# Kernel tuning notes

Measured on AMD Instinct MI355X. Metric: run time of the kernel, lower is better.

Reference implementation:

```python
import jax, jax.numpy as jnp
import numpy as np

WSIZE = (12, 12)
NUM_HEADS = 12
HEAD_DIM = 64


def _rel_idx(ws):
    wh, ww = ws
    num_dist = (2 * wh - 1) * (2 * ww - 1) + 3
    coords = np.stack(np.meshgrid(np.arange(wh), np.arange(ww), indexing='ij'))
    coords = coords.reshape(2, -1)                       # [2, wh*ww]
    rel = (coords[:, :, None] - coords[:, None, :]).transpose(1, 2, 0)
    rel[:, :, 0] += wh - 1
    rel[:, :, 1] += ww - 1
    rel[:, :, 0] *= 2 * ww - 1
    idx = np.zeros((wh * ww + 1,) * 2, dtype=np.int32)
    idx[1:, 1:] = rel.sum(-1)
    idx[0, 0:] = num_dist - 3
    idx[0:, 0] = num_dist - 2
    idx[0, 0] = num_dist - 1
    return idx.flatten()                                  # [(wh*ww+1)**2]

REL_IDX = jnp.asarray(_rel_idx(WSIZE))


def setup_inputs() -> dict:
    key = jax.random.key(0)
    ks = jax.random.split(key, 8)
    B, S, D = 1024, WSIZE[0] * WSIZE[1] + 1, NUM_HEADS * HEAD_DIM
    num_dist = (2 * WSIZE[0] - 1) * (2 * WSIZE[1] - 1) + 3
    return {
        'x': jax.random.normal(ks[0], (B, S, D), jnp.float32),
        'attn_mask': jax.random.normal(ks[1], (B, 1, S, S), jnp.float32),
        'Wq': jax.random.normal(ks[2], (D, D), jnp.float32) * 0.02,
        'bq': jnp.zeros((D,), jnp.float32),
        'Wk': jax.random.normal(ks[3], (D, D), jnp.float32) * 0.02,
        'Wv': jax.random.normal(ks[4], (D, D), jnp.float32) * 0.02,
        'bv': jnp.zeros((D,), jnp.float32),
        'rel_bias_tbl': jax.random.normal(ks[5], (num_dist, NUM_HEADS), jnp.float32) * 0.02,
    }


def reference(x, attn_mask, Wq, bq, Wk, Wv, bv, rel_bias_tbl):
    B, S, _ = x.shape
    H, D = NUM_HEADS, HEAD_DIM

    def heads(e):  # [B,S,H*D] -> [B,H,S,D]
        return e.reshape(B, S, H, D).transpose(0, 2, 1, 3)

    q = heads(x @ Wq + bq)
    k = heads(x @ Wk)            # key has no bias
    v = heads(x @ Wv + bv)

    scores = jnp.einsum('bhqd,bhkd->bhqk', q, k) / np.sqrt(D).astype(x.dtype)
    scores = scores + attn_mask
    # relative position bias: gather [S*S, H] -> [S,S,H] -> [1,H,S,S]
    rel_bias = rel_bias_tbl[REL_IDX].reshape(S, S, H).transpose(2, 0, 1)[None]
    scores = scores + rel_bias

    probs = jax.nn.softmax(scores, axis=-1)
    ctx = jnp.einsum('bhqk,bhkd->bhqd', probs, v)          # [B,H,S,D]
    return ctx.transpose(0, 2, 1, 3).reshape(B, S, H * D)
```

## Files before the change

### kernel.cpp

```cpp
#include <hip/hip_runtime.h>
#include <hip/hip_bf16.h>

typedef __bf16 bf16x8 __attribute__((ext_vector_type(8)));
typedef float f32x4 __attribute__((ext_vector_type(4)));
typedef float f32x4u __attribute__((ext_vector_type(4), aligned(4)));

#define NH 12
#define HD 64
#define SEQ 145
#define SP 160
#define DMODEL 768
#define NTOT 2304
#define BDIM 1024
#define RBS 148

__device__ __forceinline__ ushort f2bf(float f) {
  union { float f; uint u; } a; a.f = f;
  uint u = a.u;
  return (ushort)((u + 0x7FFFu + ((u >> 16) & 1u)) >> 16);
}

__device__ __forceinline__ int relidx(int qi, int ki) {
  if (ki == 0) return (qi == 0) ? 531 : 530;
  if (qi == 0) return 529;
  int q = qi - 1, k = ki - 1;
  int qh = q / 12, qw = q - qh * 12;
  int kh = k / 12, kw = k - kh * 12;
  return (qh - kh + 11) * 23 + (qw - kw + 11);
}

__device__ __forceinline__ void gload_lds16(const ushort* g, ushort* l) {
  __builtin_amdgcn_global_load_lds(
      (const __attribute__((address_space(1))) void*)g,
      (__attribute__((address_space(3))) void*)l, 16, 0, 0);
}

#define VMCNT(n) do { asm volatile("s_waitcnt vmcnt(" #n ")" ::: "memory"); \
                      __builtin_amdgcn_sched_barrier(0); } while (0)

__global__ void prep_w(const float* __restrict__ Wq, const float* __restrict__ Wk,
                       const float* __restrict__ Wv, ushort* __restrict__ Wt) {
  int i = blockIdx.x * 256 + threadIdx.x;
  if (i >= NTOT * DMODEL) return;
  int n = i / DMODEL, k = i - n * DMODEL;
  const float* W = (n < DMODEL) ? Wq : (n < 2 * DMODEL ? Wk : Wv);
  int c = n % DMODEL;
  Wt[i] = f2bf(W[k * DMODEL + c]);
}

__global__ void x2bf(const float* __restrict__ x, ushort* __restrict__ xb) {
  const size_t total = (size_t)BDIM * SEQ * DMODEL;
  size_t i = ((size_t)blockIdx.x * 256 + threadIdx.x) * 8;
  if (i >= total) return;
  float4 a = *reinterpret_cast<const float4*>(x + i);
  float4 c = *reinterpret_cast<const float4*>(x + i + 4);
  uint4 o;
  o.x = (uint)f2bf(a.x) | ((uint)f2bf(a.y) << 16);
  o.y = (uint)f2bf(a.z) | ((uint)f2bf(a.w) << 16);
  o.z = (uint)f2bf(c.x) | ((uint)f2bf(c.y) << 16);
  o.w = (uint)f2bf(c.z) | ((uint)f2bf(c.w) << 16);
  *reinterpret_cast<uint4*>(xb + i) = o;
}

__global__ void zero_vpad(ushort* __restrict__ vbuf) {
  int i = blockIdx.x * 256 + threadIdx.x;
  const int total = BDIM * NH * HD * (SP - SEQ);
  if (i >= total) return;
  int s = SEQ + i % (SP - SEQ);
  int row = i / (SP - SEQ);
  vbuf[(size_t)row * SP + s] = 0;
}

__global__ void rel_prep(const float* __restrict__ tbl, float* __restrict__ rbias) {
  int i = blockIdx.x * 256 + threadIdx.x;
  if (i >= NH * SEQ * RBS) return;
  int h = i / (SEQ * RBS);
  int rem = i - h * SEQ * RBS;
  int qi = rem / RBS, ki = rem - qi * RBS;
  rbias[i] = (ki < SEQ) ? tbl[relidx(qi, ki) * NH + h] : 0.f;
}

#define GNT 9
#define GNWG 10440
#define NKT 24

__global__ __launch_bounds__(512, 4)
void qkv_gemm(const ushort* __restrict__ xb, const ushort* __restrict__ Wt,
              const float* __restrict__ bq, const float* __restrict__ bv,
              ushort* __restrict__ qbuf, ushort* __restrict__ kbuf,
              ushort* __restrict__ vbuf) {
  __shared__ __align__(16) ushort lds[36864];

  int bid = blockIdx.x;
  int logical = (bid & 7) * 1305 + (bid >> 3);
  int mt = logical / GNT, nt = logical - (logical / GNT) * GNT;
  int m0 = mt * 128, n0 = nt * 256;

  int tid = threadIdx.x;
  int l = tid & 63, w = tid >> 6;
  int wm = w >> 2, wn = w & 3;
  int l15 = l & 15, l4 = l >> 4;
  int rslot = l4 ^ ((l15 >> 1) & 3);

  int srow = tid >> 2;
  int schunk = (tid & 3) ^ ((tid >> 3) & 3);
  const ushort* aSrc  = xb + (size_t)(m0 + srow) * DMODEL + schunk * 8;
  const ushort* bSrc0 = Wt + (size_t)(n0 + srow) * DMODEL + schunk * 8;
  const ushort* bSrc1 = Wt + (size_t)(n0 + 128 + srow) * DMODEL + schunk * 8;
  int wdst = w << 9;

#define STAGE(db, kof) do { \
    gload_lds16(aSrc  + (kof), &lds[(db) * 4096 + wdst]); \
    gload_lds16(bSrc0 + (kof), &lds[12288 + (db) * 8192 + wdst]); \
    gload_lds16(bSrc1 + (kof), &lds[12288 + (db) * 8192 + 4096 + wdst]); \
  } while (0)

  f32x4 acc[4][4];
  #pragma unroll
  for (int m = 0; m < 4; m++)
    #pragma unroll
    for (int n = 0; n < 4; n++)
      #pragma unroll
      for (int e = 0; e < 4; e++) acc[m][n][e] = 0.f;

  bf16x8 af[4], bfv[4];

#define LOADFRAG(db) do { \
    int ab_ = (db) * 4096, bb_ = 12288 + (db) * 8192; \
    _Pragma("unroll") \
    for (int i_ = 0; i_ < 4; i_++) \
      af[i_] = *reinterpret_cast<const bf16x8*>( \
          &lds[ab_ + ((wm * 64 + i_ * 16 + l15) << 5) + rslot * 8]); \
    _Pragma("unroll") \
    for (int n_ = 0; n_ < 4; n_++) \
      bfv[n_] = *reinterpret_cast<const bf16x8*>( \
          &lds[bb_ + ((wn * 64 + n_ * 16 + l15) << 5) + rslot * 8]); \
  } while (0)
#define MFMA16() do { \
    __builtin_amdgcn_s_setprio(1); \
    _Pragma("unroll") \
    for (int i_ = 0; i_ < 4; i_++) \
      _Pragma("unroll") \
      for (int n_ = 0; n_ < 4; n_++) \
        acc[i_][n_] = __builtin_amdgcn_mfma_f32_16x16x32_bf16( \
            af[i_], bfv[n_], acc[i_][n_], 0, 0, 0); \
    __builtin_amdgcn_s_setprio(0); \
  } while (0)

  STAGE(0, 0);
  STAGE(1, 32);
  VMCNT(3);
  __builtin_amdgcn_s_barrier();

  #pragma unroll
  for (int t = 0; t < NKT; ++t) {
    int cur = t % 3, nx2 = (t + 2) % 3;
    if (t + 2 < NKT) STAGE(nx2, (t + 2) * 32);
    LOADFRAG(cur);
    MFMA16();
    if (t < NKT - 1) {
      if (t + 2 < NKT) { VMCNT(3); }
      else             { VMCNT(0); }
      __builtin_amdgcn_s_barrier();
    }
  }

  int which = n0 / DMODEL;
  int h_[4], dh_[4];
  float bias_[4];
  #pragma unroll
  for (int nn = 0; nn < 4; nn++) {
    int col = n0 + wn * 64 + nn * 16 + l15;
    int hcol = col - which * DMODEL;
    h_[nn] = hcol >> 6; dh_[nn] = hcol & 63;
    bias_[nn] = (which == 0) ? bq[hcol] : (which == 2 ? bv[hcol] : 0.f);
  }

  if (which != 2) {
    #pragma unroll
    for (int i = 0; i < 4; i++) {
      #pragma unroll
      for (int r = 0; r < 4; r++) {
        int row = m0 + wm * 64 + i * 16 + (l4 << 2) + r;
        int b = row / SEQ;
        int s = row - b * SEQ;
        #pragma unroll
        for (int nn = 0; nn < 4; nn++) {
          float v = acc[i][nn][r] + bias_[nn];
          size_t bh = (size_t)b * NH + h_[nn];
          if (which == 0) {
            v *= 0.125f;
            qbuf[(bh * SEQ + s) * HD + dh_[nn]] = f2bf(v);
          } else {
            kbuf[(bh * SEQ + s) * HD + dh_[nn]] = f2bf(v);
          }
        }
      }
    }
  } else {
    __syncthreads();
    ushort* T = &lds[w * 4608];
    #pragma unroll
    for (int i = 0; i < 4; i++) {
      #pragma unroll
      for (int nn = 0; nn < 4; nn++) {
        int cl = nn * 16 + l15;
        int rl = i * 16 + (l4 << 2);
        ushort4 pk;
        pk.x = f2bf(acc[i][nn][0] + bias_[nn]);
        pk.y = f2bf(acc[i][nn][1] + bias_[nn]);
        pk.z = f2bf(acc[i][nn][2] + bias_[nn]);
        pk.w = f2bf(acc[i][nn][3] + bias_[nn]);
        *reinterpret_cast<ushort4*>(&T[cl * 72 + rl]) = pk;
      }
    }
    asm volatile("s_waitcnt lgkmcnt(0)" ::: "memory");
    __builtin_amdgcn_sched_barrier(0);
    int hU = ((n0 - 2 * DMODEL) >> 6) + wn;
    int rowbase = m0 + wm * 64;
    #pragma unroll
    for (int c = 0; c < 8; c++) {
      uint4 vv = *reinterpret_cast<const uint4*>(&T[l * 72 + c * 8]);
      int R = rowbase + c * 8;
      int b0 = R / SEQ;
      int b7 = (R + 7) / SEQ;
      if (b0 == b7) {
        int s0 = R - b0 * SEQ;
        size_t addr = (((size_t)b0 * NH + hU) * HD + l) * SP + s0;
        *reinterpret_cast<uint4*>(vbuf + addr) = vv;
      } else {
        const ushort* pv = reinterpret_cast<const ushort*>(&vv);
        #pragma unroll
        for (int e = 0; e < 8; e++) {
          int row = R + e;
          int bb = row / SEQ, ss = row - bb * SEQ;
          vbuf[(((size_t)bb * NH + hU) * HD + l) * SP + ss] = pv[e];
        }
      }
    }
  }
#undef STAGE
#undef LOADFRAG
#undef MFMA16
}

#define AH 4
__global__ __launch_bounds__(256, 2)
void attn_kernel(const ushort* __restrict__ qbuf, const ushort* __restrict__ kbuf,
                 const ushort* __restrict__ vbuf, const float* __restrict__ mask,
                 const float* __restrict__ rbias, float* __restrict__ out) {
  __shared__ __align__(16) ushort plds[AH][16][SP + 8];

  int id = blockIdx.x;
  int xcd = id & 7;
  int j = id >> 3;
  int b = xcd + 8 * (j / 3);
  int hg = j % 3;

  int tid = threadIdx.x;
  int lane = tid & 63, w = tid >> 6;
  int h = hg * AH + w;
  int l15 = lane & 15, l4 = lane >> 4;
  int bh = b * NH + h;

  const ushort* qp = qbuf + (size_t)bh * SEQ * HD;
  const ushort* kp = kbuf + (size_t)bh * SEQ * HD;
  const ushort* vp = vbuf + (size_t)bh * HD * SP;
  const float* mbase = mask + (size_t)b * SEQ * SEQ;
  const float* rbase = rbias + (size_t)h * SEQ * RBS;

  uint4 kfa[10], kfb[10];
  #pragma unroll
  for (int ct = 0; ct < 5; ct++) {
    int krow = ct * 16 + l15;
    kfa[2 * ct]     = *reinterpret_cast<const uint4*>(kp + krow * HD + l4 * 8);
    kfa[2 * ct + 1] = *reinterpret_cast<const uint4*>(kp + krow * HD + 32 + l4 * 8);
  }
  #pragma unroll
  for (int ct = 5; ct < 10; ct++) {
    int krow = ct * 16 + l15;
    if (krow >= SEQ) krow = 0;
    kfb[2 * (ct - 5)]     = *reinterpret_cast<const uint4*>(kp + krow * HD + l4 * 8);
    kfb[2 * (ct - 5) + 1] = *reinterpret_cast<const uint4*>(kp + krow * HD + 32 + l4 * 8);
  }
  uint4 vba[10], vbb[10];
  #pragma unroll
  for (int t = 0; t < 10; t++) {
    int ntl = t / 5, ks = t % 5;
    vba[t] = *reinterpret_cast<const uint4*>(
        vp + (ntl * 16 + l15) * SP + ks * 32 + l4 * 8);
  }
  #pragma unroll
  for (int t = 0; t < 10; t++) {
    int ntl = 2 + t / 5, ks = t % 5;
    vbb[t] = *reinterpret_cast<const uint4*>(
        vp + (ntl * 16 + l15) * SP + ks * 32 + l4 * 8);
  }

  #pragma unroll 1
  for (int strip = 0; strip < 10; strip++) {
    int r0 = strip * 16;
    int qi = r0 + l15;
    int qc = (qi < SEQ) ? qi : (SEQ - 1);
    bool qok = (qi < SEQ);
    const float* mrow = mbase + (size_t)qc * SEQ;
    const float* rp = rbase + (size_t)qc * RBS;

    bf16x8 qf0, qf1;
    if (qok) {
      qf0 = *reinterpret_cast<const bf16x8*>(qp + qi * HD + l4 * 8);
      qf1 = *reinterpret_cast<const bf16x8*>(qp + qi * HD + 32 + l4 * 8);
    } else {
      uint4 z = make_uint4(0, 0, 0, 0);
      qf0 = *reinterpret_cast<bf16x8*>(&z);
      qf1 = *reinterpret_cast<bf16x8*>(&z);
    }

    f32x4 sc[10];
    #pragma unroll
    for (int ct = 0; ct < 9; ct++) {
      int kb = ct * 16 + l4 * 4;
      f32x4u rb = *reinterpret_cast<const f32x4u*>(rp + kb);
      f32x4u mk = *reinterpret_cast<const f32x4u*>(mrow + kb);
      #pragma unroll
      for (int r = 0; r < 4; r++)
        sc[ct][r] = qok ? (mk[r] + rb[r]) : -3e38f;
    }
    {
      float iv = (l4 == 0 && qok) ? (mrow[144] + rp[144]) : -3e38f;
      sc[9][0] = iv; sc[9][1] = -3e38f; sc[9][2] = -3e38f; sc[9][3] = -3e38f;
    }

    #pragma unroll
    for (int ct = 0; ct < 5; ct++) {
      sc[ct] = __builtin_amdgcn_mfma_f32_16x16x32_bf16(
          *reinterpret_cast<bf16x8*>(&kfa[2 * ct]), qf0, sc[ct], 0, 0, 0);
      sc[ct] = __builtin_amdgcn_mfma_f32_16x16x32_bf16(
          *reinterpret_cast<bf16x8*>(&kfa[2 * ct + 1]), qf1, sc[ct], 0, 0, 0);
    }
    #pragma unroll
    for (int ct = 5; ct < 10; ct++) {
      sc[ct] = __builtin_amdgcn_mfma_f32_16x16x32_bf16(
          *reinterpret_cast<bf16x8*>(&kfb[2 * (ct - 5)]), qf0, sc[ct], 0, 0, 0);
      sc[ct] = __builtin_amdgcn_mfma_f32_16x16x32_bf16(
          *reinterpret_cast<bf16x8*>(&kfb[2 * (ct - 5) + 1]), qf1, sc[ct], 0, 0, 0);
    }

    float mx = -3e38f;
    #pragma unroll
    for (int ct = 0; ct < 10; ct++)
      #pragma unroll
      for (int r = 0; r < 4; r++) mx = fmaxf(mx, sc[ct][r]);
    mx = fmaxf(mx, __shfl_xor(mx, 16, 64));
    mx = fmaxf(mx, __shfl_xor(mx, 32, 64));
    float sum = 0.f;
    #pragma unroll
    for (int ct = 0; ct < 10; ct++)
      #pragma unroll
      for (int r = 0; r < 4; r++) {
        float p = __expf(sc[ct][r] - mx);
        sc[ct][r] = p;
        sum += p;
      }
    sum += __shfl_xor(sum, 16, 64);
    sum += __shfl_xor(sum, 32, 64);
    float inv = 1.f / sum;

    #pragma unroll
    for (int ct = 0; ct < 10; ct++) {
      ushort4 pk;
      pk.x = f2bf(sc[ct][0] * inv);
      pk.y = f2bf(sc[ct][1] * inv);
      pk.z = f2bf(sc[ct][2] * inv);
      pk.w = f2bf(sc[ct][3] * inv);
      *reinterpret_cast<ushort4*>(&plds[w][l15][ct * 16 + l4 * 4]) = pk;
    }

    #pragma unroll
    for (int ntl = 0; ntl < 2; ntl++) {
      f32x4 pacc;
      #pragma unroll
      for (int e = 0; e < 4; e++) pacc[e] = 0.f;
      #pragma unroll
      for (int ks = 0; ks < 5; ks++) {
        bf16x8 pa = *reinterpret_cast<const bf16x8*>(
            &plds[w][l15][ks * 32 + l4 * 8]);
        pacc = __builtin_amdgcn_mfma_f32_16x16x32_bf16(
            pa, *reinterpret_cast<bf16x8*>(&vba[ntl * 5 + ks]), pacc, 0, 0, 0);
      }
      #pragma unroll
      for (int r = 0; r < 4; r++) {
        int s = r0 + l4 * 4 + r;
        if (s < SEQ)
          out[((size_t)b * SEQ + s) * DMODEL + h * HD + ntl * 16 + l15] = pacc[r];
      }
    }
    #pragma unroll
    for (int ntl = 2; ntl < 4; ntl++) {
      f32x4 pacc;
      #pragma unroll
      for (int e = 0; e < 4; e++) pacc[e] = 0.f;
      #pragma unroll
      for (int ks = 0; ks < 5; ks++) {
        bf16x8 pa = *reinterpret_cast<const bf16x8*>(
            &plds[w][l15][ks * 32 + l4 * 8]);
        pacc = __builtin_amdgcn_mfma_f32_16x16x32_bf16(
            pa, *reinterpret_cast<bf16x8*>(&vbb[(ntl - 2) * 5 + ks]), pacc, 0, 0, 0);
      }
      #pragma unroll
      for (int r = 0; r < 4; r++) {
        int s = r0 + l4 * 4 + r;
        if (s < SEQ)
          out[((size_t)b * SEQ + s) * DMODEL + h * HD + ntl * 16 + l15] = pacc[r];
      }
    }
  }
}

extern "C" void kernel_launch(void* const* d_in, const int* in_sizes, int n_in,
                              void* d_out, int out_size, void* d_ws, size_t ws_size,
                              hipStream_t stream) {
  const float* x    = (const float*)d_in[0];
  const float* mask = (const float*)d_in[1];
  const float* Wq   = (const float*)d_in[2];
  const float* bq   = (const float*)d_in[3];
  const float* Wk   = (const float*)d_in[4];
  const float* Wv   = (const float*)d_in[5];
  const float* bv   = (const float*)d_in[6];
  const float* tbl  = (const float*)d_in[7];
  float* out = (float*)d_out;

  char* ws = (char*)d_ws;
  ushort* Wt = (ushort*)ws;
  size_t off = (size_t)NTOT * DMODEL * 2;
  ushort* qbuf = (ushort*)(ws + off); off += (size_t)BDIM * NH * SEQ * HD * 2;
  ushort* kbuf = (ushort*)(ws + off); off += (size_t)BDIM * NH * SEQ * HD * 2;
  ushort* vbuf = (ushort*)(ws + off); off += (size_t)BDIM * NH * HD * SP * 2;
  float*  rbias = (float*)(ws + off); off += (size_t)NH * SEQ * RBS * 4 + 64;

  ushort* xbuf = (ushort*)d_out;

  prep_w<<<(NTOT * DMODEL + 255) / 256, 256, 0, stream>>>(Wq, Wk, Wv, Wt);
  zero_vpad<<<(BDIM * NH * HD * (SP - SEQ) + 255) / 256, 256, 0, stream>>>(vbuf);
  rel_prep<<<(NH * SEQ * RBS + 255) / 256, 256, 0, stream>>>(tbl, rbias);
  {
    size_t total = (size_t)BDIM * SEQ * DMODEL;
    x2bf<<<(int)(total / 8 / 256), 256, 0, stream>>>(x, xbuf);
  }

  qkv_gemm<<<GNWG, 512, 0, stream>>>(xbuf, Wt, bq, bv, qbuf, kbuf, vbuf);

  attn_kernel<<<BDIM * 3, 256, 0, stream>>>(qbuf, kbuf, vbuf, mask, rbias, out);
}
```

Before: 1.231 ms.

## Fuse fp32-to-bf16 conversion of x into the QKV GEMM A-tile loader

Removes the separate x2bf kernel and has the QKV GEMM read fp32 x directly. Each A tile is loaded into registers, converted to bf16 and written to LDS, double-buffered in registers across iterations, while B still uses direct global-to-LDS loads. This saves a full pass that writes and rereads the bf16 copy of x. In exchange, A is read as fp32 by each of the 9 N-tiles, doubling A traffic per workgroup, and the pipeline gains extra register pressure and an LDS wait before each barrier.

```diff
diff --git a/kernel.cpp b/kernel.cpp
--- a/kernel.cpp
+++ b/kernel.cpp
@@ -20,6 +20,10 @@
   return (ushort)((u + 0x7FFFu + ((u >> 16) & 1u)) >> 16);
 }
 
+__device__ __forceinline__ uint pk2(float lo, float hi) {
+  return (uint)f2bf(lo) | ((uint)f2bf(hi) << 16);
+}
+
 __device__ __forceinline__ int relidx(int qi, int ki) {
   if (ki == 0) return (qi == 0) ? 531 : 530;
   if (qi == 0) return 529;
@@ -37,6 +41,8 @@
 
 #define VMCNT(n) do { asm volatile("s_waitcnt vmcnt(" #n ")" ::: "memory"); \
                       __builtin_amdgcn_sched_barrier(0); } while (0)
+#define LGKM0 do { asm volatile("s_waitcnt lgkmcnt(0)" ::: "memory"); \
+                   __builtin_amdgcn_sched_barrier(0); } while (0)
 
 __global__ void prep_w(const float* __restrict__ Wq, const float* __restrict__ Wk,
                        const float* __restrict__ Wv, ushort* __restrict__ Wt) {
@@ -48,20 +54,6 @@
   Wt[i] = f2bf(W[k * DMODEL + c]);
 }
 
-__global__ void x2bf(const float* __restrict__ x, ushort* __restrict__ xb) {
-  const size_t total = (size_t)BDIM * SEQ * DMODEL;
-  size_t i = ((size_t)blockIdx.x * 256 + threadIdx.x) * 8;
-  if (i >= total) return;
-  float4 a = *reinterpret_cast<const float4*>(x + i);
-  float4 c = *reinterpret_cast<const float4*>(x + i + 4);
-  uint4 o;
-  o.x = (uint)f2bf(a.x) | ((uint)f2bf(a.y) << 16);
-  o.y = (uint)f2bf(a.z) | ((uint)f2bf(a.w) << 16);
-  o.z = (uint)f2bf(c.x) | ((uint)f2bf(c.y) << 16);
-  o.w = (uint)f2bf(c.z) | ((uint)f2bf(c.w) << 16);
-  *reinterpret_cast<uint4*>(xb + i) = o;
-}
-
 __global__ void zero_vpad(ushort* __restrict__ vbuf) {
   int i = blockIdx.x * 256 + threadIdx.x;
   const int total = BDIM * NH * HD * (SP - SEQ);
@@ -85,7 +77,7 @@
 #define NKT 24
 
 __global__ __launch_bounds__(512, 4)
-void qkv_gemm(const ushort* __restrict__ xb, const ushort* __restrict__ Wt,
+void qkv_gemm(const float* __restrict__ x, const ushort* __restrict__ Wt,
               const float* __restrict__ bq, const float* __restrict__ bv,
               ushort* __restrict__ qbuf, ushort* __restrict__ kbuf,
               ushort* __restrict__ vbuf) {
@@ -102,15 +94,26 @@
   int l15 = l & 15, l4 = l >> 4;
   int rslot = l4 ^ ((l15 >> 1) & 3);
 
-  int srow = tid >> 2;
+  int arow = tid >> 2;
+  const float* xf = x + (size_t)(m0 + arow) * DMODEL + (tid & 3) * 8;
+  int awaddr = (arow << 5) + (((tid & 3) ^ ((tid >> 3) & 3)) << 3);
+
   int schunk = (tid & 3) ^ ((tid >> 3) & 3);
-  const ushort* aSrc  = xb + (size_t)(m0 + srow) * DMODEL + schunk * 8;
-  const ushort* bSrc0 = Wt + (size_t)(n0 + srow) * DMODEL + schunk * 8;
-  const ushort* bSrc1 = Wt + (size_t)(n0 + 128 + srow) * DMODEL + schunk * 8;
+  const ushort* bSrc0 = Wt + (size_t)(n0 + arow) * DMODEL + schunk * 8;
+  const ushort* bSrc1 = Wt + (size_t)(n0 + 128 + arow) * DMODEL + schunk * 8;
   int wdst = w << 9;
 
-#define STAGE(db, kof) do { \
-    gload_lds16(aSrc  + (kof), &lds[(db) * 4096 + wdst]); \
+#define ALOAD(s0, s1, kof) do { \
+    s0 = *reinterpret_cast<const float4*>(xf + (kof)); \
+    s1 = *reinterpret_cast<const float4*>(xf + (kof) + 4); \
+  } while (0)
+#define ACVTW(db, s0, s1) do { \
+    uint4 o_; \
+    o_.x = pk2(s0.x, s0.y); o_.y = pk2(s0.z, s0.w); \
+    o_.z = pk2(s1.x, s1.y); o_.w = pk2(s1.z, s1.w); \
+    *reinterpret_cast<uint4*>(&lds[(db) * 4096 + awaddr]) = o_; \
+  } while (0)
+#define STAGE_B(db, kof) do { \
     gload_lds16(bSrc0 + (kof), &lds[12288 + (db) * 8192 + wdst]); \
     gload_lds16(bSrc1 + (kof), &lds[12288 + (db) * 8192 + 4096 + wdst]); \
   } while (0)
@@ -147,20 +150,33 @@
     __builtin_amdgcn_s_setprio(0); \
   } while (0)
 
-  STAGE(0, 0);
-  STAGE(1, 32);
-  VMCNT(3);
+  float4 aE0, aE1, aO0, aO1;
+
+  ALOAD(aE0, aE1, 0);
+  STAGE_B(0, 0);
+  ALOAD(aO0, aO1, 32);
+  STAGE_B(1, 32);
+  VMCNT(4);
+  ACVTW(0, aE0, aE1);
+  LGKM0;
   __builtin_amdgcn_s_barrier();
 
   #pragma unroll
   for (int t = 0; t < NKT; ++t) {
-    int cur = t % 3, nx2 = (t + 2) % 3;
-    if (t + 2 < NKT) STAGE(nx2, (t + 2) * 32);
-    LOADFRAG(cur);
+    if (t + 2 < NKT) {
+      if ((t & 1) == 0) ALOAD(aE0, aE1, (t + 2) * 32);
+      else              ALOAD(aO0, aO1, (t + 2) * 32);
+      STAGE_B((t + 2) % 3, (t + 2) * 32);
+    }
+    if (t + 1 < NKT) {
+      if (t + 2 < NKT) { VMCNT(4); } else { VMCNT(0); }
+      if ((t & 1) == 0) ACVTW((t + 1) % 3, aO0, aO1);
+      else              ACVTW((t + 1) % 3, aE0, aE1);
+    }
+    LOADFRAG(t % 3);
     MFMA16();
     if (t < NKT - 1) {
-      if (t + 2 < NKT) { VMCNT(3); }
-      else             { VMCNT(0); }
+      LGKM0;
       __builtin_amdgcn_s_barrier();
     }
   }
@@ -214,8 +230,7 @@
         *reinterpret_cast<ushort4*>(&T[cl * 72 + rl]) = pk;
       }
     }
-    asm volatile("s_waitcnt lgkmcnt(0)" ::: "memory");
-    __builtin_amdgcn_sched_barrier(0);
+    LGKM0;
     int hU = ((n0 - 2 * DMODEL) >> 6) + wn;
     int rowbase = m0 + wm * 64;
     #pragma unroll
@@ -239,7 +254,9 @@
       }
     }
   }
-#undef STAGE
+#undef ALOAD
+#undef ACVTW
+#undef STAGE_B
 #undef LOADFRAG
 #undef MFMA16
 }
@@ -438,17 +455,11 @@
   ushort* vbuf = (ushort*)(ws + off); off += (size_t)BDIM * NH * HD * SP * 2;
   float*  rbias = (float*)(ws + off); off += (size_t)NH * SEQ * RBS * 4 + 64;
 
-  ushort* xbuf = (ushort*)d_out;
-
   prep_w<<<(NTOT * DMODEL + 255) / 256, 256, 0, stream>>>(Wq, Wk, Wv, Wt);
   zero_vpad<<<(BDIM * NH * HD * (SP - SEQ) + 255) / 256, 256, 0, stream>>>(vbuf);
   rel_prep<<<(NH * SEQ * RBS + 255) / 256, 256, 0, stream>>>(tbl, rbias);
-  {
-    size_t total = (size_t)BDIM * SEQ * DMODEL;
-    x2bf<<<(int)(total / 8 / 256), 256, 0, stream>>>(x, xbuf);
-  }
-
-  qkv_gemm<<<GNWG, 512, 0, stream>>>(xbuf, Wt, bq, bv, qbuf, kbuf, vbuf);
+
+  qkv_gemm<<<GNWG, 512, 0, stream>>>(x, Wt, bq, bv, qbuf, kbuf, vbuf);
 
   attn_kernel<<<BDIM * 3, 256, 0, stream>>>(qbuf, kbuf, vbuf, mask, rbias, out);
 }
```

Result: slower. 1.344 ms (+9.2%).

## Merge prep kernels and stage Q/K epilogue through LDS for 16-byte stores

Applied to the files above, without the earlier changes.

Merges the weight transpose, V-padding zeroing and relative-bias table prep into one launch to cut kernel launch overhead. The Q/K GEMM epilogue now writes bf16 results into per-wave LDS tiles and then issues coalesced 16-byte global stores of 8 consecutive head-dim elements, replacing scattered 2-byte stores. This adds a block barrier and LDS traffic before the epilogue for all tiles.

```diff
diff --git a/kernel.cpp b/kernel.cpp
--- a/kernel.cpp
+++ b/kernel.cpp
@@ -38,14 +38,35 @@
 #define VMCNT(n) do { asm volatile("s_waitcnt vmcnt(" #n ")" ::: "memory"); \
                       __builtin_amdgcn_sched_barrier(0); } while (0)
 
-__global__ void prep_w(const float* __restrict__ Wq, const float* __restrict__ Wk,
-                       const float* __restrict__ Wv, ushort* __restrict__ Wt) {
-  int i = blockIdx.x * 256 + threadIdx.x;
-  if (i >= NTOT * DMODEL) return;
-  int n = i / DMODEL, k = i - n * DMODEL;
-  const float* W = (n < DMODEL) ? Wq : (n < 2 * DMODEL ? Wk : Wv);
-  int c = n % DMODEL;
-  Wt[i] = f2bf(W[k * DMODEL + c]);
+#define NP1 6912
+#define NP2 46080
+#define NP3 1006
+__global__ void prep_all(const float* __restrict__ Wq, const float* __restrict__ Wk,
+                         const float* __restrict__ Wv, ushort* __restrict__ Wt,
+                         ushort* __restrict__ vbuf, const float* __restrict__ tbl,
+                         float* __restrict__ rbias) {
+  int bid = blockIdx.x;
+  int tid = threadIdx.x;
+  if (bid < NP1) {
+    int i = bid * 256 + tid;
+    int n = i / DMODEL, k = i - n * DMODEL;
+    const float* W = (n < DMODEL) ? Wq : (n < 2 * DMODEL ? Wk : Wv);
+    int c = n % DMODEL;
+    Wt[i] = f2bf(W[k * DMODEL + c]);
+  } else if (bid < NP1 + NP2) {
+    int i = (bid - NP1) * 256 + tid;
+    int s = SEQ + i % (SP - SEQ);
+    int row = i / (SP - SEQ);
+    vbuf[(size_t)row * SP + s] = 0;
+  } else {
+    int i = (bid - NP1 - NP2) * 256 + tid;
+    if (i < NH * SEQ * RBS) {
+      int h = i / (SEQ * RBS);
+      int rem = i - h * SEQ * RBS;
+      int qi = rem / RBS, ki = rem - qi * RBS;
+      rbias[i] = (ki < SEQ) ? tbl[relidx(qi, ki) * NH + h] : 0.f;
+    }
+  }
 }
 
 __global__ void x2bf(const float* __restrict__ x, ushort* __restrict__ xb) {
@@ -60,24 +81,6 @@
   o.z = (uint)f2bf(c.x) | ((uint)f2bf(c.y) << 16);
   o.w = (uint)f2bf(c.z) | ((uint)f2bf(c.w) << 16);
   *reinterpret_cast<uint4*>(xb + i) = o;
-}
-
-__global__ void zero_vpad(ushort* __restrict__ vbuf) {
-  int i = blockIdx.x * 256 + threadIdx.x;
-  const int total = BDIM * NH * HD * (SP - SEQ);
-  if (i >= total) return;
-  int s = SEQ + i % (SP - SEQ);
-  int row = i / (SP - SEQ);
-  vbuf[(size_t)row * SP + s] = 0;
-}
-
-__global__ void rel_prep(const float* __restrict__ tbl, float* __restrict__ rbias) {
-  int i = blockIdx.x * 256 + threadIdx.x;
-  if (i >= NH * SEQ * RBS) return;
-  int h = i / (SEQ * RBS);
-  int rem = i - h * SEQ * RBS;
-  int qi = rem / RBS, ki = rem - qi * RBS;
-  rbias[i] = (ki < SEQ) ? tbl[relidx(qi, ki) * NH + h] : 0.f;
 }
 
 #define GNT 9
@@ -166,40 +169,43 @@
   }
 
   int which = n0 / DMODEL;
-  int h_[4], dh_[4];
   float bias_[4];
   #pragma unroll
   for (int nn = 0; nn < 4; nn++) {
     int col = n0 + wn * 64 + nn * 16 + l15;
     int hcol = col - which * DMODEL;
-    h_[nn] = hcol >> 6; dh_[nn] = hcol & 63;
     bias_[nn] = (which == 0) ? bq[hcol] : (which == 2 ? bv[hcol] : 0.f);
   }
+  int hU = ((n0 - which * DMODEL) >> 6) + wn;
+  int rowbase = m0 + wm * 64;
+
+  __syncthreads();
+  ushort* T = &lds[w * 4608];
 
   if (which != 2) {
-    #pragma unroll
-    for (int i = 0; i < 4; i++) {
-      #pragma unroll
-      for (int r = 0; r < 4; r++) {
-        int row = m0 + wm * 64 + i * 16 + (l4 << 2) + r;
-        int b = row / SEQ;
-        int s = row - b * SEQ;
+    float scale = (which == 0) ? 0.125f : 1.f;
+    #pragma unroll
+    for (int i = 0; i < 4; i++)
+      #pragma unroll
+      for (int nn = 0; nn < 4; nn++)
         #pragma unroll
-        for (int nn = 0; nn < 4; nn++) {
-          float v = acc[i][nn][r] + bias_[nn];
-          size_t bh = (size_t)b * NH + h_[nn];
-          if (which == 0) {
-            v *= 0.125f;
-            qbuf[(bh * SEQ + s) * HD + dh_[nn]] = f2bf(v);
-          } else {
-            kbuf[(bh * SEQ + s) * HD + dh_[nn]] = f2bf(v);
-          }
-        }
-      }
+        for (int r = 0; r < 4; r++)
+          T[(i * 16 + (l4 << 2) + r) * 72 + nn * 16 + l15] =
+              f2bf((acc[i][nn][r] + bias_[nn]) * scale);
+    asm volatile("s_waitcnt lgkmcnt(0)" ::: "memory");
+    __builtin_amdgcn_sched_barrier(0);
+    ushort* dst = (which == 0) ? qbuf : kbuf;
+    int chunk = l & 7;
+    #pragma unroll
+    for (int c = 0; c < 8; c++) {
+      int rl = (l >> 3) + 8 * c;
+      uint4 vv = *reinterpret_cast<const uint4*>(&T[rl * 72 + chunk * 8]);
+      int row = rowbase + rl;
+      int bb = row / SEQ, ss = row - bb * SEQ;
+      size_t addr = (((size_t)bb * NH + hU) * SEQ + ss) * HD + chunk * 8;
+      *reinterpret_cast<uint4*>(dst + addr) = vv;
     }
   } else {
-    __syncthreads();
-    ushort* T = &lds[w * 4608];
     #pragma unroll
     for (int i = 0; i < 4; i++) {
       #pragma unroll
@@ -216,8 +222,6 @@
     }
     asm volatile("s_waitcnt lgkmcnt(0)" ::: "memory");
     __builtin_amdgcn_sched_barrier(0);
-    int hU = ((n0 - 2 * DMODEL) >> 6) + wn;
-    int rowbase = m0 + wm * 64;
     #pragma unroll
     for (int c = 0; c < 8; c++) {
       uint4 vv = *reinterpret_cast<const uint4*>(&T[l * 72 + c * 8]);
@@ -440,9 +444,7 @@
 
   ushort* xbuf = (ushort*)d_out;
 
-  prep_w<<<(NTOT * DMODEL + 255) / 256, 256, 0, stream>>>(Wq, Wk, Wv, Wt);
-  zero_vpad<<<(BDIM * NH * HD * (SP - SEQ) + 255) / 256, 256, 0, stream>>>(vbuf);
-  rel_prep<<<(NH * SEQ * RBS + 255) / 256, 256, 0, stream>>>(tbl, rbias);
+  prep_all<<<NP1 + NP2 + NP3, 256, 0, stream>>>(Wq, Wk, Wv, Wt, vbuf, tbl, rbias);
   {
     size_t total = (size_t)BDIM * SEQ * DMODEL;
     x2bf<<<(int)(total / 8 / 256), 256, 0, stream>>>(x, xbuf);
```

New measurement: 1.200 ms. 2.6% less time.
